# Performance work log

Hardware: AMD Instinct MI355X
Metric: run time of the kernel (lower is better)

## Reference

```python
import jax, jax.numpy as jnp
import numpy as np

NEG_INF = -1e9
B, Q, M, D, H = 8, 512, 512, 1024, 16
S = D // H  # size per head


def rel_shift(x):
    # x: [B, H, Q, R] -> TransformerXL relative shift
    b, h, q, r = x.shape
    x = jnp.pad(x, ((0, 0), (0, 0), (0, 0), (1, 0)))
    x = x.reshape(b, h, r + 1, q)[:, :, 1:, :]
    return x.reshape(b, h, q, r)


def setup_inputs() -> dict:
    key = jax.random.key(0)
    ks = jax.random.split(key, 10)
    query_seqs = jax.random.normal(ks[0], (B, Q, D), jnp.float32)
    memory_seqs = jax.random.normal(ks[1], (B, M, D), jnp.float32)
    positional_encoding = jax.random.normal(ks[2], (Q + M, D), jnp.float32)
    # causal mask over concatenated [memory | query]: query token i may attend
    # to all memory tokens and query tokens <= i. 1 = masked.
    q_idx = jnp.arange(Q)[:, None]
    r_idx = jnp.arange(Q + M)[None, :]
    token_mask = (r_idx > q_idx + M).astype(jnp.float32)[None, None]  # [1,1,Q,Q+M]
    std = 0.02
    Wq = jax.random.normal(ks[3], (D, H, S), jnp.float32) * std
    Wk = jax.random.normal(ks[4], (D, H, S), jnp.float32) * std
    Wv = jax.random.normal(ks[5], (D, H, S), jnp.float32) * std
    Wr = jax.random.normal(ks[6], (D, H, S), jnp.float32) * std
    Wo = jax.random.normal(ks[7], (H, S, D), jnp.float32) * std
    content_bias = jax.random.normal(ks[8], (H, S), jnp.float32) * std
    position_bias = jax.random.normal(ks[9], (H, S), jnp.float32) * std
    return dict(query_seqs=query_seqs, memory_seqs=memory_seqs,
                positional_encoding=positional_encoding, token_mask=token_mask,
                Wq=Wq, Wk=Wk, Wv=Wv, Wr=Wr, Wo=Wo,
                content_bias=content_bias, position_bias=position_bias)


def reference(query_seqs, memory_seqs, positional_encoding, token_mask,
              Wq, Wk, Wv, Wr, Wo, content_bias, position_bias):
    # reference = [memory | query] along time axis
    reference_seqs = jnp.concatenate([memory_seqs, query_seqs], axis=1)  # [B,R,D]
    q = jnp.einsum('bqd,dhs->bqhs', query_seqs, Wq)       # [B,Q,H,S]
    k = jnp.einsum('brd,dhs->brhs', reference_seqs, Wk)   # [B,R,H,S]
    v = jnp.einsum('brd,dhs->brhs', reference_seqs, Wv)   # [B,R,H,S]
    r = jnp.einsum('rd,dhs->rhs', positional_encoding, Wr)  # [R,H,S]

    content = jnp.einsum('bqhs,brhs->bhqr', q + content_bias, k)
    positions = jnp.einsum('bqhs,rhs->bhqr', q + position_bias, r)
    positions = rel_shift(positions)

    logits = (content + positions) / jnp.sqrt(jnp.float32(S))
    logits = logits + token_mask * NEG_INF
    attn = jax.nn.softmax(logits, axis=3)  # dropout disabled (inference)

    out = jnp.einsum('bhqr,brhs->bqhs', attn, v)
    return jnp.einsum('bqhs,hsd->bqd', out, Wo)
```

## Files before the change

kernel.cpp:

```cpp
#include <hip/hip_runtime.h>

typedef _Float16 f16;
typedef _Float16 f16x8 __attribute__((ext_vector_type(8)));
typedef float f32x4 __attribute__((ext_vector_type(4)));

#define MFMA_F16(a, b, c) __builtin_amdgcn_mfma_f32_16x16x32_f16((a), (b), (c), 0, 0, 0)

#define SCL 0.125f

__device__ __forceinline__ void gl_lds16(const void* g, void* l) {
    __builtin_amdgcn_global_load_lds((const __attribute__((address_space(1))) unsigned int*)g,
                                     (__attribute__((address_space(3))) unsigned int*)l, 16, 0, 0);
}

__global__ void prep(const float* __restrict__ q, const float* __restrict__ mem,
                     const float* __restrict__ Wq, const float* __restrict__ Wk,
                     const float* __restrict__ Wv, const float* __restrict__ Wr,
                     const float* __restrict__ Wo,
                     f16* __restrict__ wt, f16* __restrict__ ref16)
{
    __shared__ float t[32][33];
    const int bid = blockIdx.x, tid = threadIdx.x;
    if (bid < 5120) {
        const int wi = bid >> 10, tt = bid & 1023;
        const float* src;
        switch (wi) { case 0: src = Wq; break; case 1: src = Wk; break;
                      case 2: src = Wv; break; case 3: src = Wr; break; default: src = Wo; }
        f16* dst = wt + ((size_t)wi << 20);
        const int x = (tt & 31) * 32, y = (tt >> 5) * 32;
        const int tx = tid & 31, ty = tid >> 5;
#pragma unroll
        for (int k2 = 0; k2 < 4; ++k2)
            t[ty + k2 * 8][tx] = src[(size_t)(y + ty + k2 * 8) * 1024 + x + tx];
        __syncthreads();
#pragma unroll
        for (int k2 = 0; k2 < 4; ++k2)
            dst[(size_t)(x + ty + k2 * 8) * 1024 + y + tx] = (f16)t[tx][ty + k2 * 8];
    } else {
        const int idx = (bid - 5120) * 256 + tid;
        const int half = idx >> 19;
        const int c = idx & 0x7FFFF;
        const int b = c >> 16, i = (c >> 7) & 511, ch = c & 127;
        const float* src = (half == 0 ? q : mem) + (((size_t)(b * 512 + i)) << 10) + ch * 8;
        const int t2 = (half == 0) ? (512 + i) : i;
        f16* dst = ref16 + ((((size_t)b << 10) + t2) << 10) + ch * 8;
        const float4 f0 = reinterpret_cast<const float4*>(src)[0];
        const float4 f1 = reinterpret_cast<const float4*>(src)[1];
        f16x8 v;
        v[0] = (f16)f0.x; v[1] = (f16)f0.y; v[2] = (f16)f0.z; v[3] = (f16)f0.w;
        v[4] = (f16)f1.x; v[5] = (f16)f1.y; v[6] = (f16)f1.z; v[7] = (f16)f1.w;
        *reinterpret_cast<f16x8*>(dst) = v;
    }
}

__global__ __launch_bounds__(512, 2)
void proj_kernel(const f16* __restrict__ ref16, const float* __restrict__ posenc,
                 const f16* __restrict__ wts,
                 f16* __restrict__ qc16, f16* __restrict__ qp16,
                 f16* __restrict__ k16, f16* __restrict__ vT16, f16* __restrict__ r16,
                 const float* __restrict__ cb, const float* __restrict__ pbias)
{
    __shared__ __align__(16) f16 SH[40960];
    f16* At = SH;
    f16* Bk = SH + 8192;
    f16* Bv = SH + 24576;

    const int tid = threadIdx.x, lane = tid & 63, w = tid >> 6;
    const int wr = w >> 2, wc = w & 3;

    const int bid = blockIdx.x;
    int mode, local, perx, shf;
    if (bid < 256)      { mode = 0; local = bid;       perx = 8; shf = 3; }
    else if (bid < 384) { mode = 1; local = bid - 256; perx = 4; shf = 2; }
    else                { mode = 2; local = bid - 384; perx = 1; shf = 0; }
    const int xcd = local & 7, m = local >> 3;
    const int rt = xcd * perx + (m & (perx - 1));
    const int ct = m >> shf;
    const int i0 = rt * 128, n0 = ct * 256;
    const f16* BT0 = (mode == 0) ? wts + (1u << 20) : (mode == 1) ? wts : wts + (3u << 20);
    const f16* BTv = wts + (2u << 20);

    f32x4 acck[4][4] = {};
    f32x4 accv[4][4] = {};

    for (int ks = 0; ks < 16; ++ks) {
        const int k0 = ks * 64;
#pragma unroll
        for (int it = 0; it < 2; ++it) {
            const int c = tid + it * 512;
            const int row = c >> 3, ch = c & 7, chs = ch ^ (row & 7);
            const int grow = i0 + row;
            if (mode == 2) {
                const float* sr = posenc + (size_t)grow * 1024 + k0 + ch * 8;
                const float4 f0 = reinterpret_cast<const float4*>(sr)[0];
                const float4 f1 = reinterpret_cast<const float4*>(sr)[1];
                f16x8 av;
                av[0] = (f16)f0.x; av[1] = (f16)f0.y; av[2] = (f16)f0.z; av[3] = (f16)f0.w;
                av[4] = (f16)f1.x; av[5] = (f16)f1.y; av[6] = (f16)f1.z; av[7] = (f16)f1.w;
                *reinterpret_cast<f16x8*>(reinterpret_cast<char*>(At) + row * 128 + (chs << 4)) = av;
            } else {
                const size_t arow = (mode == 1) ? (size_t)((grow >> 9) * 1024 + 512 + (grow & 511))
                                                : (size_t)grow;
                gl_lds16(ref16 + arow * 1024 + k0 + chs * 8,
                         reinterpret_cast<char*>(At) + ((c & ~63) << 4));
            }
        }
#pragma unroll
        for (int it = 0; it < 4; ++it) {
            const int c = tid + it * 512;
            const int row = c >> 3, ch = c & 7, chs = ch ^ (row & 7);
            gl_lds16(BT0 + (size_t)(n0 + row) * 1024 + k0 + chs * 8,
                     reinterpret_cast<char*>(Bk) + ((c & ~63) << 4));
        }
        if (mode == 0) {
#pragma unroll
            for (int it = 0; it < 4; ++it) {
                const int c = tid + it * 512;
                const int row = c >> 3, ch = c & 7, chs = ch ^ (row & 7);
                gl_lds16(BTv + (size_t)(n0 + row) * 1024 + k0 + chs * 8,
                         reinterpret_cast<char*>(Bv) + ((c & ~63) << 4));
            }
        }
        __syncthreads();
#pragma unroll
        for (int kk = 0; kk < 2; ++kk) {
            f16x8 avf[4], bkf[4];
            const int chh = kk * 4 + (lane >> 4);
#pragma unroll
            for (int mi = 0; mi < 4; ++mi) {
                const int row = wr * 64 + mi * 16 + (lane & 15);
                avf[mi] = *reinterpret_cast<const f16x8*>(reinterpret_cast<char*>(At) + row * 128 + ((chh ^ (row & 7)) << 4));
            }
#pragma unroll
            for (int n = 0; n < 4; ++n) {
                const int row = wc * 64 + n * 16 + (lane & 15);
                bkf[n] = *reinterpret_cast<const f16x8*>(reinterpret_cast<char*>(Bk) + row * 128 + ((chh ^ (row & 7)) << 4));
            }
#pragma unroll
            for (int mi = 0; mi < 4; ++mi)
#pragma unroll
                for (int n = 0; n < 4; ++n)
                    acck[mi][n] = MFMA_F16(avf[mi], bkf[n], acck[mi][n]);
            if (mode == 0) {
                f16x8 bvf[4];
#pragma unroll
                for (int n = 0; n < 4; ++n) {
                    const int row = wc * 64 + n * 16 + (lane & 15);
                    bvf[n] = *reinterpret_cast<const f16x8*>(reinterpret_cast<char*>(Bv) + row * 128 + ((chh ^ (row & 7)) << 4));
                }
#pragma unroll
                for (int mi = 0; mi < 4; ++mi)
#pragma unroll
                    for (int n = 0; n < 4; ++n)
                        accv[mi][n] = MFMA_F16(avf[mi], bvf[n], accv[mi][n]);
            }
        }
        __syncthreads();
    }

    if (mode == 0) {
#pragma unroll
        for (int mi = 0; mi < 4; ++mi)
#pragma unroll
            for (int n = 0; n < 4; ++n)
#pragma unroll
                for (int rg = 0; rg < 4; ++rg) {
                    const int row = i0 + wr * 64 + mi * 16 + (lane >> 4) * 4 + rg;
                    const int col = n0 + wc * 64 + n * 16 + (lane & 15);
                    const int b = row >> 10, j = row & 1023, h = col >> 6, s = col & 63;
                    k16[(((size_t)(b * 16 + h) * 1024) + j) * 64 + s] = (f16)acck[mi][n][rg];
                }
        const int b = i0 >> 10;
        const int j0l = i0 & 1023;
#pragma unroll
        for (int hf = 0; hf < 2; ++hf) {
            if ((wc >> 1) == hf) {
#pragma unroll
                for (int mi = 0; mi < 4; ++mi)
#pragma unroll
                    for (int n = 0; n < 4; ++n)
#pragma unroll
                        for (int rg = 0; rg < 4; ++rg) {
                            const int jl = wr * 64 + mi * 16 + (lane >> 4) * 4 + rg;
                            const int cl = (wc & 1) * 64 + n * 16 + (lane & 15);
                            SH[cl * 128 + jl] = (f16)accv[mi][n][rg];
                        }
            }
            __syncthreads();
#pragma unroll
            for (int it = 0; it < 4; ++it) {
                const int c = tid + it * 512;
                const int cl = c >> 4, ch = c & 15;
                const int col = n0 + hf * 128 + cl;
                const int h = col >> 6, s = col & 63;
                f16* dst = vT16 + (((size_t)(b * 16 + h) * 64 + s) * 1024 + j0l + ch * 8);
                *reinterpret_cast<f16x8*>(dst) = *reinterpret_cast<const f16x8*>(SH + cl * 128 + ch * 8);
            }
            __syncthreads();
        }
    } else {
#pragma unroll
        for (int mi = 0; mi < 4; ++mi)
#pragma unroll
            for (int n = 0; n < 4; ++n)
#pragma unroll
                for (int rg = 0; rg < 4; ++rg) {
                    const int row = i0 + wr * 64 + mi * 16 + (lane >> 4) * 4 + rg;
                    const int col = n0 + wc * 64 + n * 16 + (lane & 15);
                    const float v = acck[mi][n][rg];
                    if (mode == 1) {
                        const int b = row >> 9, i = row & 511, h = col >> 6, s = col & 63;
                        const size_t idx = (((size_t)(b * 16 + h) * 512) + i) * 64 + s;
                        qc16[idx] = (f16)((v + cb[col]) * SCL);
                        qp16[idx] = (f16)((v + pbias[col]) * SCL);
                    } else {
                        const int h = col >> 6, s = col & 63;
                        r16[((size_t)h * 1024 + row) * 64 + s] = (f16)v;
                    }
                }
    }
}

__global__ __launch_bounds__(512, 4)
void oproj_kernel(const f16* __restrict__ ao16, const f16* __restrict__ WoT, float* __restrict__ out)
{
    __shared__ __align__(16) f16 SH[24576];
    f16* At = SH;
    f16* Bt = SH + 8192;
    const int tid = threadIdx.x, lane = tid & 63, w = tid >> 6;
    const int wr = w >> 2, wc = w & 3;
    const int xcd = blockIdx.x & 7, m = blockIdx.x >> 3;
    const int rt = xcd * 4 + (m & 3), ct = m >> 2;
    const int i0 = rt * 128, n0 = ct * 256;

    f32x4 acc[4][4] = {};
    for (int ks = 0; ks < 16; ++ks) {
        const int k0 = ks * 64;
#pragma unroll
        for (int it = 0; it < 2; ++it) {
            const int c = tid + it * 512;
            const int row = c >> 3, ch = c & 7, chs = ch ^ (row & 7);
            gl_lds16(ao16 + (size_t)(i0 + row) * 1024 + k0 + chs * 8,
                     reinterpret_cast<char*>(At) + ((c & ~63) << 4));
        }
#pragma unroll
        for (int it = 0; it < 4; ++it) {
            const int c = tid + it * 512;
            const int row = c >> 3, ch = c & 7, chs = ch ^ (row & 7);
            gl_lds16(WoT + (size_t)(n0 + row) * 1024 + k0 + chs * 8,
                     reinterpret_cast<char*>(Bt) + ((c & ~63) << 4));
        }
        __syncthreads();
#pragma unroll
        for (int kk = 0; kk < 2; ++kk) {
            f16x8 avf[4], bvf[4];
            const int chh = kk * 4 + (lane >> 4);
#pragma unroll
            for (int mi = 0; mi < 4; ++mi) {
                const int row = wr * 64 + mi * 16 + (lane & 15);
                avf[mi] = *reinterpret_cast<const f16x8*>(reinterpret_cast<char*>(At) + row * 128 + ((chh ^ (row & 7)) << 4));
            }
#pragma unroll
            for (int n = 0; n < 4; ++n) {
                const int row = wc * 64 + n * 16 + (lane & 15);
                bvf[n] = *reinterpret_cast<const f16x8*>(reinterpret_cast<char*>(Bt) + row * 128 + ((chh ^ (row & 7)) << 4));
            }
#pragma unroll
            for (int mi = 0; mi < 4; ++mi)
#pragma unroll
                for (int n = 0; n < 4; ++n)
                    acc[mi][n] = MFMA_F16(avf[mi], bvf[n], acc[mi][n]);
        }
        __syncthreads();
    }
#pragma unroll
    for (int mi = 0; mi < 4; ++mi)
#pragma unroll
        for (int n = 0; n < 4; ++n)
#pragma unroll
            for (int rg = 0; rg < 4; ++rg) {
                const int row = i0 + wr * 64 + mi * 16 + (lane >> 4) * 4 + rg;
                const int col = n0 + wc * 64 + n * 16 + (lane & 15);
                out[(size_t)row * 1024 + col] = acc[mi][n][rg];
            }
}

__global__ __launch_bounds__(512, 4)
void attn_kernel(const f16* __restrict__ qc16, const f16* __restrict__ qp16,
                 const f16* __restrict__ k16, const f16* __restrict__ vT16,
                 const f16* __restrict__ r16, f16* __restrict__ attnout)
{
    __shared__ __align__(16) f16 KT[4096], VT[4096], RT[4096];
    __shared__ __align__(16) f16 PR[128 * 68];
    __shared__ __align__(16) f16 PB[8 * 2 * 16 * 68];

    const int tid = threadIdx.x, lane = tid & 63, w = tid >> 6;
    const int n = blockIdx.x;
    const int xcd = n & 7, m = n >> 3;
    const int h = xcd + 8 * (m >> 5);
    const int b = (m >> 2) & 7;
    const int iB = m & 3;
    const int i0 = iB * 128;
    const int bh = b * 16 + h;

    const f16* kbase = k16 + (size_t)bh * 1024 * 64;
    const f16* vbase = vT16 + (size_t)bh * 64 * 1024;
    const f16* rbase = r16 + (size_t)h * 1024 * 64;

    f16x8 qcf[2], qpf[2];
    {
        const size_t qoff = ((size_t)bh * 512 + i0 + w * 16 + (lane & 15)) * 64;
#pragma unroll
        for (int kk = 0; kk < 2; ++kk) {
            const int ch = (kk * 4 + (lane >> 4)) * 8;
            qcf[kk] = *reinterpret_cast<const f16x8*>(qc16 + qoff + ch);
            qpf[kk] = *reinterpret_cast<const f16x8*>(qp16 + qoff + ch);
        }
    }

    auto stage64 = [&](f16* dst, const f16* src, int rowstride) {
        const int row = tid >> 3, ch = tid & 7, chs = ch ^ (row & 7);
        gl_lds16(src + (size_t)row * rowstride + chs * 8,
                 reinterpret_cast<char*>(dst) + ((tid & ~63) << 4));
    };

    auto compute_pblock = [&](int bt) {
        const int slot = bt & 1;
        f32x4 pc[4] = {};
#pragma unroll
        for (int kk = 0; kk < 2; ++kk) {
            const int chh = kk * 4 + (lane >> 4);
#pragma unroll
            for (int tf = 0; tf < 4; ++tf) {
                const int brow = tf * 16 + (lane & 15);
                const f16x8 rv = *reinterpret_cast<const f16x8*>(reinterpret_cast<char*>(RT) + brow * 128 + ((chh ^ (brow & 7)) << 4));
                pc[tf] = MFMA_F16(qpf[kk], rv, pc[tf]);
            }
        }
        f16* pbw = PB + (size_t)((w * 2 + slot) * 16) * 68;
#pragma unroll
        for (int tf = 0; tf < 4; ++tf)
#pragma unroll
            for (int rg = 0; rg < 4; ++rg) {
                const int r = (lane >> 4) * 4 + rg;
                pbw[r * 68 + tf * 16 + (lane & 15)] = (f16)pc[tf][rg];
            }
    };

    {
        const int bt0 = 6 - 2 * iB;
        stage64(RT, rbase + (size_t)(bt0 * 64) * 64, 64);
        __syncthreads();
        compute_pblock(bt0);
        __syncthreads();
        stage64(RT, rbase + (size_t)((bt0 + 1) * 64) * 64, 64);
        __syncthreads();
        compute_pblock(bt0 + 1);
    }

    float mrun[4] = {-1e30f, -1e30f, -1e30f, -1e30f};
    float lrun[4] = {0.f, 0.f, 0.f, 0.f};
    f32x4 o[4] = {};

    const int njt = 2 * iB + 10;
    for (int jt = 0; jt < njt; ++jt) {
        const int j0 = jt * 64;
        const int bt = jt - 2 * iB + 8;
        __syncthreads();
        stage64(KT, kbase + (size_t)j0 * 64, 64);
        stage64(VT, vbase + j0, 1024);
        if (bt <= 15) stage64(RT, rbase + (size_t)(bt * 64) * 64, 64);
        __syncthreads();

        if (w < 4 && bt <= 15) compute_pblock(bt);

        f32x4 cfr[4] = {};
        __builtin_amdgcn_s_setprio(1);
#pragma unroll
        for (int kk = 0; kk < 2; ++kk) {
            const int chh = kk * 4 + (lane >> 4);
#pragma unroll
            for (int jf = 0; jf < 4; ++jf) {
                const int brow = jf * 16 + (lane & 15);
                const f16x8 kv = *reinterpret_cast<const f16x8*>(reinterpret_cast<char*>(KT) + brow * 128 + ((chh ^ (brow & 7)) << 4));
                cfr[jf] = MFMA_F16(qcf[kk], kv, cfr[jf]);
            }
        }
        __builtin_amdgcn_s_setprio(0);

        const int tb = j0 + 511 - i0 - w * 16;
        float lg[4][4];
#pragma unroll
        for (int jf = 0; jf < 4; ++jf)
#pragma unroll
            for (int rg = 0; rg < 4; ++rg) {
                const int il = (lane >> 4) * 4 + rg;
                const int t = tb + jf * 16 + (lane & 15) - il;
                const float pv = (float)PB[(size_t)((w * 2 + ((t >> 6) & 1)) * 16 + il) * 68 + (t & 63)];
                lg[jf][rg] = (t <= 1023) ? (cfr[jf][rg] + pv) : -1e30f;
            }

        float mx[4];
#pragma unroll
        for (int rg = 0; rg < 4; ++rg) {
            float v = fmaxf(fmaxf(lg[0][rg], lg[1][rg]), fmaxf(lg[2][rg], lg[3][rg]));
#pragma unroll
            for (int d = 1; d < 16; d <<= 1) v = fmaxf(v, __shfl_xor(v, d));
            mx[rg] = v;
        }
        const float need = fmaxf(fmaxf(mx[0] - mrun[0], mx[1] - mrun[1]),
                                 fmaxf(mx[2] - mrun[2], mx[3] - mrun[3]));
        if (__all(need <= 8.0f)) {
#pragma unroll
            for (int rg = 0; rg < 4; ++rg) {
                float rs = 0.f;
                const int il = w * 16 + (lane >> 4) * 4 + rg;
#pragma unroll
                for (int jf = 0; jf < 4; ++jf) {
                    const float p = __expf(lg[jf][rg] - mrun[rg]);
                    rs += p;
                    PR[il * 68 + jf * 16 + (lane & 15)] = (f16)p;
                }
#pragma unroll
                for (int d = 1; d < 16; d <<= 1) rs += __shfl_xor(rs, d);
                lrun[rg] += rs;
            }
        } else {
#pragma unroll
            for (int rg = 0; rg < 4; ++rg) {
                const float mnew = fmaxf(mrun[rg], mx[rg]);
                const float al = __expf(mrun[rg] - mnew);
                mrun[rg] = mnew;
                float rs = 0.f;
                const int il = w * 16 + (lane >> 4) * 4 + rg;
#pragma unroll
                for (int jf = 0; jf < 4; ++jf) {
                    const float p = __expf(lg[jf][rg] - mnew);
                    rs += p;
                    PR[il * 68 + jf * 16 + (lane & 15)] = (f16)p;
                }
#pragma unroll
                for (int d = 1; d < 16; d <<= 1) rs += __shfl_xor(rs, d);
                lrun[rg] = lrun[rg] * al + rs;
#pragma unroll
                for (int sf = 0; sf < 4; ++sf) o[sf][rg] *= al;
            }
        }

        __builtin_amdgcn_s_setprio(1);
#pragma unroll
        for (int kk = 0; kk < 2; ++kk) {
            const int chh = kk * 4 + (lane >> 4);
            const int arow = w * 16 + (lane & 15);
            const f16x8 ap = *reinterpret_cast<const f16x8*>(reinterpret_cast<char*>(PR) + arow * 136 + chh * 16);
#pragma unroll
            for (int sf = 0; sf < 4; ++sf) {
                const int brow = sf * 16 + (lane & 15);
                const f16x8 vv = *reinterpret_cast<const f16x8*>(reinterpret_cast<char*>(VT) + brow * 128 + ((chh ^ (brow & 7)) << 4));
                o[sf] = MFMA_F16(ap, vv, o[sf]);
            }
        }
        __builtin_amdgcn_s_setprio(0);

        if (w >= 4 && bt <= 15) compute_pblock(bt);
    }

#pragma unroll
    for (int sf = 0; sf < 4; ++sf)
#pragma unroll
        for (int rg = 0; rg < 4; ++rg) {
            const int il = w * 16 + (lane >> 4) * 4 + rg;
            const int row = b * 512 + i0 + il;
            const int col = h * 64 + sf * 16 + (lane & 15);
            attnout[(size_t)row * 1024 + col] = (f16)(o[sf][rg] / lrun[rg]);
        }
}

extern "C" void kernel_launch(void* const* d_in, const int* in_sizes, int n_in,
                              void* d_out, int out_size, void* d_ws, size_t ws_size,
                              hipStream_t stream)
{
    const float* query = (const float*)d_in[0];
    const float* memory = (const float*)d_in[1];
    const float* posenc = (const float*)d_in[2];
    const float* Wq = (const float*)d_in[4];
    const float* Wk = (const float*)d_in[5];
    const float* Wv = (const float*)d_in[6];
    const float* Wr = (const float*)d_in[7];
    const float* Wo = (const float*)d_in[8];
    const float* cb = (const float*)d_in[9];
    const float* pb = (const float*)d_in[10];
    float* out = (float*)d_out;

    if (ws_size < (size_t)38 * (1u << 20) * sizeof(f16)) return;
    f16* ws = (f16*)d_ws;
    f16* WoT = ws + (4u << 20);
    f16* ref16 = ws + (5u << 20);
    f16* ao16 = ref16;
    f16* qc16 = ref16 + (8u << 20);
    f16* qp16 = qc16 + (4u << 20);
    f16* k16 = qp16 + (4u << 20);
    f16* vT16 = k16 + (8u << 20);
    f16* r16 = vT16 + (8u << 20);

    prep<<<9216, 256, 0, stream>>>(query, memory, Wq, Wk, Wv, Wr, Wo, ws, ref16);
    proj_kernel<<<416, 512, 0, stream>>>(ref16, posenc, ws, qc16, qp16, k16, vT16, r16, cb, pb);
    attn_kernel<<<512, 512, 0, stream>>>(qc16, qp16, k16, vT16, r16, ao16);
    oproj_kernel<<<128, 512, 0, stream>>>(ao16, WoT, out);
}
```

Baseline: 196.6 us.

## Triple-buffer output projection with async LDS prefetch and tune occupancy bounds

The output projection GEMM moves from a single staged buffer with two block barriers per k-step to a three-slot LDS ring. Loads for step ks+2 are issued between the fragment reads and the MFMAs, and explicit vmcnt waits with one barrier per step replace the old synchronisation. The aim is to hide global-to-LDS latency behind compute, at the cost of tripled LDS use, so oproj occupancy bounds drop from 4 to 2 blocks. Separately, proj_kernel gets a 4-block launch bound, which may cause register spills, and its V transpose buffer gets a padded stride to reduce LDS bank conflicts.

```diff
diff --git a/kernel.cpp b/kernel.cpp
--- a/kernel.cpp
+++ b/kernel.cpp
@@ -7,6 +7,9 @@
 #define MFMA_F16(a, b, c) __builtin_amdgcn_mfma_f32_16x16x32_f16((a), (b), (c), 0, 0, 0)
 
 #define SCL 0.125f
+
+#define VM_WAIT6 asm volatile("s_waitcnt vmcnt(6)" ::: "memory")
+#define VM_WAIT0 asm volatile("s_waitcnt vmcnt(0)" ::: "memory")
 
 __device__ __forceinline__ void gl_lds16(const void* g, void* l) {
     __builtin_amdgcn_global_load_lds((const __attribute__((address_space(1))) unsigned int*)g,
@@ -53,7 +56,7 @@
     }
 }
 
-__global__ __launch_bounds__(512, 2)
+__global__ __launch_bounds__(512, 4)
 void proj_kernel(const f16* __restrict__ ref16, const float* __restrict__ posenc,
                  const f16* __restrict__ wts,
                  f16* __restrict__ qc16, f16* __restrict__ qp16,
@@ -183,7 +186,7 @@
                         for (int rg = 0; rg < 4; ++rg) {
                             const int jl = wr * 64 + mi * 16 + (lane >> 4) * 4 + rg;
                             const int cl = (wc & 1) * 64 + n * 16 + (lane & 15);
-                            SH[cl * 128 + jl] = (f16)accv[mi][n][rg];
+                            SH[cl * 132 + jl] = (f16)accv[mi][n][rg];
                         }
             }
             __syncthreads();
@@ -194,7 +197,7 @@
                 const int col = n0 + hf * 128 + cl;
                 const int h = col >> 6, s = col & 63;
                 f16* dst = vT16 + (((size_t)(b * 16 + h) * 64 + s) * 1024 + j0l + ch * 8);
-                *reinterpret_cast<f16x8*>(dst) = *reinterpret_cast<const f16x8*>(SH + cl * 128 + ch * 8);
+                *reinterpret_cast<f16x8*>(dst) = *reinterpret_cast<const f16x8*>(SH + cl * 132 + ch * 8);
             }
             __syncthreads();
         }
@@ -221,12 +224,10 @@
     }
 }
 
-__global__ __launch_bounds__(512, 4)
+__global__ __launch_bounds__(512, 2)
 void oproj_kernel(const f16* __restrict__ ao16, const f16* __restrict__ WoT, float* __restrict__ out)
 {
-    __shared__ __align__(16) f16 SH[24576];
-    f16* At = SH;
-    f16* Bt = SH + 8192;
+    __shared__ __align__(16) f16 SH[3 * 24576];
     const int tid = threadIdx.x, lane = tid & 63, w = tid >> 6;
     const int wr = w >> 2, wc = w & 3;
     const int xcd = blockIdx.x & 7, m = blockIdx.x >> 3;
@@ -234,23 +235,44 @@
     const int i0 = rt * 128, n0 = ct * 256;
 
     f32x4 acc[4][4] = {};
-    for (int ks = 0; ks < 16; ++ks) {
+
+    auto stage_part = [&](int ks, int slot, int part) {
         const int k0 = ks * 64;
-#pragma unroll
-        for (int it = 0; it < 2; ++it) {
-            const int c = tid + it * 512;
-            const int row = c >> 3, ch = c & 7, chs = ch ^ (row & 7);
-            gl_lds16(ao16 + (size_t)(i0 + row) * 1024 + k0 + chs * 8,
-                     reinterpret_cast<char*>(At) + ((c & ~63) << 4));
-        }
-#pragma unroll
-        for (int it = 0; it < 4; ++it) {
-            const int c = tid + it * 512;
+        f16* At = SH + slot * 24576;
+        f16* Bt = At + 8192;
+        if (part == 0) {
+#pragma unroll
+            for (int it = 0; it < 2; ++it) {
+                const int c = tid + it * 512;
+                const int row = c >> 3, ch = c & 7, chs = ch ^ (row & 7);
+                gl_lds16(ao16 + (size_t)(i0 + row) * 1024 + k0 + chs * 8,
+                         reinterpret_cast<char*>(At) + ((c & ~63) << 4));
+            }
+            const int c = tid;
             const int row = c >> 3, ch = c & 7, chs = ch ^ (row & 7);
             gl_lds16(WoT + (size_t)(n0 + row) * 1024 + k0 + chs * 8,
                      reinterpret_cast<char*>(Bt) + ((c & ~63) << 4));
-        }
-        __syncthreads();
+        } else {
+#pragma unroll
+            for (int it = 1; it < 4; ++it) {
+                const int c = tid + it * 512;
+                const int row = c >> 3, ch = c & 7, chs = ch ^ (row & 7);
+                gl_lds16(WoT + (size_t)(n0 + row) * 1024 + k0 + chs * 8,
+                         reinterpret_cast<char*>(Bt) + ((c & ~63) << 4));
+            }
+        }
+    };
+
+    stage_part(0, 0, 0); stage_part(0, 0, 1);
+    stage_part(1, 1, 0); stage_part(1, 1, 1);
+    for (int ks = 0; ks < 16; ++ks) {
+        const int cur = ks % 3;
+        const int s2 = (ks + 2) % 3;
+        f16* At = SH + cur * 24576;
+        f16* Bt = At + 8192;
+        if (ks < 15) { VM_WAIT6; } else { VM_WAIT0; }
+        __builtin_amdgcn_sched_barrier(0);
+        __builtin_amdgcn_s_barrier();
 #pragma unroll
         for (int kk = 0; kk < 2; ++kk) {
             f16x8 avf[4], bvf[4];
@@ -265,14 +287,16 @@
                 const int row = wc * 64 + n * 16 + (lane & 15);
                 bvf[n] = *reinterpret_cast<const f16x8*>(reinterpret_cast<char*>(Bt) + row * 128 + ((chh ^ (row & 7)) << 4));
             }
+            if (ks < 14) stage_part(ks + 2, s2, kk);
 #pragma unroll
             for (int mi = 0; mi < 4; ++mi)
 #pragma unroll
                 for (int n = 0; n < 4; ++n)
                     acc[mi][n] = MFMA_F16(avf[mi], bvf[n], acc[mi][n]);
-        }
-        __syncthreads();
-    }
+            __builtin_amdgcn_sched_barrier(0);
+        }
+    }
+
 #pragma unroll
     for (int mi = 0; mi < 4; ++mi)
 #pragma unroll
```

Measured after the change: 497.2 us. +152.8%, slower.
